# Kernel optimization log

Hardware: AMD Instinct MI355X
Metric: run time of the kernel (lower is better)

## Reference

```python
import jax, jax.numpy as jnp
import numpy as np

N = 100000   # relation nodes (== source nodes per scale)
D = 128      # per-scale feature size
EPS = 1e-6   # LayerNorm eps from the torch module


def setup_inputs() -> dict:
    key = jax.random.key(0)
    ks = jax.random.split(key, 10)
    inp = {}
    for i, s in enumerate(['s1', 's2', 's3', 's4']):
        inp[f'feat_{s}'] = jax.random.normal(ks[i], (N, D), dtype=jnp.float32)
        inp[f'idx_{s}'] = jax.random.randint(ks[4 + i], (N,), 0, N, dtype=jnp.int32)
    inp['W'] = jax.random.normal(ks[8], (4 * D, 4 * D), dtype=jnp.float32) * 0.04
    inp['b'] = jnp.zeros((4 * D,), dtype=jnp.float32)
    inp['gamma'] = jnp.ones((4 * D,), dtype=jnp.float32)
    inp['beta'] = jnp.zeros((4 * D,), dtype=jnp.float32)
    return inp


def reference(feat_s1, feat_s2, feat_s3, feat_s4,
              idx_s1, idx_s2, idx_s3, idx_s4,
              W, b, gamma, beta):
    # copy_src message passing per scale == gather src features to each
    # relation node (uniform in-degree 1), mailbox flatten -> [N, D] per scale.
    gathered = jnp.concatenate([
        jnp.take(feat_s1, idx_s1, axis=0),
        jnp.take(feat_s2, idx_s2, axis=0),
        jnp.take(feat_s3, idx_s3, axis=0),
        jnp.take(feat_s4, idx_s4, axis=0),
    ], axis=1)                                  # [N, 4D]
    h = gathered @ W.T + b                      # nn.Linear(4D, 4D)
    h = jax.nn.relu(h)
    # LayerNorm(4D, eps=1e-6, elementwise_affine=True)
    mu = jnp.mean(h, axis=-1, keepdims=True)
    var = jnp.mean(jnp.square(h - mu), axis=-1, keepdims=True)
    return (h - mu) * jax.lax.rsqrt(var + EPS) * gamma + beta
```

## Files before the change

### kernel.cpp

```cpp
#include <hip/hip_runtime.h>
#include <stdint.h>

#define N_ROWS 100000
#define EPS 1e-6f

typedef float f32x4 __attribute__((ext_vector_type(4)));
typedef __bf16 bf16x8 __attribute__((ext_vector_type(8)));
typedef ushort u16x8 __attribute__((ext_vector_type(8)));

__device__ __forceinline__ ushort f2bf(float f) {
  union { float f; uint32_t u; } v; v.f = f;
  uint32_t u = v.u;
  return (ushort)((u + 0x7FFFu + ((u >> 16) & 1u)) >> 16);
}

__global__ __launch_bounds__(256) void wconv2_kernel(const float* __restrict__ W,
                                                     ushort* __restrict__ Wf) {
  int t = blockIdx.x * 256 + threadIdx.x;
  int frag = t >> 6;
  int lane = t & 63;
  int j = (frag >> 4) * 16 + (lane & 15);
  int kb = (frag & 15) * 32 + (lane >> 4) * 8;
  const float* src = W + j * 512 + kb;
  float4 a = *(const float4*)src;
  float4 b = *(const float4*)(src + 4);
  ushort4 lo, hi;
  lo.x = f2bf(a.x); lo.y = f2bf(a.y); lo.z = f2bf(a.z); lo.w = f2bf(a.w);
  hi.x = f2bf(b.x); hi.y = f2bf(b.y); hi.z = f2bf(b.z); hi.w = f2bf(b.w);
  ushort* dst = Wf + (size_t)t * 8;
  *(ushort4*)dst = lo;
  *(ushort4*)(dst + 4) = hi;
}

__global__ __launch_bounds__(512, 4) void fused4_kernel(
    const float* __restrict__ f1, const float* __restrict__ f2,
    const float* __restrict__ f3, const float* __restrict__ f4,
    const int* __restrict__ i1, const int* __restrict__ i2,
    const int* __restrict__ i3, const int* __restrict__ i4,
    const ushort* __restrict__ Wf, const float* __restrict__ bias,
    const float* __restrict__ gamma, const float* __restrict__ beta,
    float* __restrict__ out) {
  __shared__ ushort Al[64 * 512];
  __shared__ float2 red[64 * 8];

  const int t = threadIdx.x;
  const int w = t >> 6;
  const int l = t & 63;
  const int cl = l & 15;
  const int gq = l >> 4;
  const int blk = blockIdx.x;

  const int arow = t >> 3;
  const int e8 = t & 7;
  int gi = blk * 64 + arow;
  int gic = gi < N_ROWS ? gi : (N_ROWS - 1);
  const float* tb0 = f1 + (size_t)i1[gic] * 128 + e8 * 8;
  const float* tb1 = f2 + (size_t)i2[gic] * 128 + e8 * 8;
  const float* tb2 = f3 + (size_t)i3[gic] * 128 + e8 * 8;
  const float* tb3 = f4 + (size_t)i4[gic] * 128 + e8 * 8;

  float4 pa[4][2], pb[4][2];
#pragma unroll
  for (int h = 0; h < 2; ++h) {
    pa[0][h] = *(const float4*)(tb0 + h * 64);
    pb[0][h] = *(const float4*)(tb0 + h * 64 + 4);
    pa[1][h] = *(const float4*)(tb1 + h * 64);
    pb[1][h] = *(const float4*)(tb1 + h * 64 + 4);
    pa[2][h] = *(const float4*)(tb2 + h * 64);
    pb[2][h] = *(const float4*)(tb2 + h * 64 + 4);
    pa[3][h] = *(const float4*)(tb3 + h * 64);
    pb[3][h] = *(const float4*)(tb3 + h * 64 + 4);
  }

#pragma unroll
  for (int T = 0; T < 4; ++T)
#pragma unroll
    for (int h = 0; h < 2; ++h) {
      u16x8 o;
      o[0] = f2bf(pa[T][h].x); o[1] = f2bf(pa[T][h].y);
      o[2] = f2bf(pa[T][h].z); o[3] = f2bf(pa[T][h].w);
      o[4] = f2bf(pb[T][h].x); o[5] = f2bf(pb[T][h].y);
      o[6] = f2bf(pb[T][h].z); o[7] = f2bf(pb[T][h].w);
      const int c = (T * 16 + h * 8 + e8) ^ (arow & 15);
      *(u16x8*)(Al + arow * 512 + c * 8) = o;
    }

  const ushort* Bbase = Wf + ((size_t)w * 4 * 16 * 64 + l) * 8;

  f32x4 acc[4][4];
#pragma unroll
  for (int rb = 0; rb < 4; ++rb)
#pragma unroll
    for (int cb = 0; cb < 4; ++cb)
      acc[rb][cb] = (f32x4){0.f, 0.f, 0.f, 0.f};

  __syncthreads();

#pragma unroll
  for (int kt = 0; kt < 16; ++kt) {
    bf16x8 bfr[4];
#pragma unroll
    for (int cb = 0; cb < 4; ++cb)
      bfr[cb] = *(const bf16x8*)(Bbase + ((size_t)cb * 16 + kt) * 512);
    bf16x8 af[4];
#pragma unroll
    for (int rb = 0; rb < 4; ++rb) {
      const int c = (kt * 4 + gq) ^ cl;
      af[rb] = *(const bf16x8*)(Al + (rb * 16 + cl) * 512 + c * 8);
    }
#pragma unroll
    for (int cb = 0; cb < 4; ++cb)
#pragma unroll
      for (int rb = 0; rb < 4; ++rb)
        acc[rb][cb] = __builtin_amdgcn_mfma_f32_16x16x32_bf16(
            af[rb], bfr[cb], acc[rb][cb], 0, 0, 0);
  }

  const int wcol = w * 64;
  float bia[4], gam[4], bet[4];
#pragma unroll
  for (int cb = 0; cb < 4; ++cb) {
    int col = wcol + cb * 16 + cl;
    bia[cb] = bias[col];
    gam[cb] = gamma[col];
    bet[cb] = beta[col];
  }

#pragma unroll
  for (int rb = 0; rb < 4; ++rb) {
#pragma unroll
    for (int r = 0; r < 4; ++r) {
      float s = 0.f, ss = 0.f;
#pragma unroll
      for (int cb = 0; cb < 4; ++cb) {
        float v = acc[rb][cb][r] + bia[cb];
        v = fmaxf(v, 0.f);
        acc[rb][cb][r] = v;
        s += v;
        ss += v * v;
      }
#pragma unroll
      for (int m = 1; m < 16; m <<= 1) {
        s += __shfl_xor(s, m);
        ss += __shfl_xor(ss, m);
      }
      if (cl == 0) {
        int row = rb * 16 + gq * 4 + r;
        red[row * 8 + w] = make_float2(s, ss);
      }
    }
  }
  __syncthreads();

#pragma unroll
  for (int rb = 0; rb < 4; ++rb) {
#pragma unroll
    for (int r = 0; r < 4; ++r) {
      int row = rb * 16 + gq * 4 + r;
      float S = 0.f, SS = 0.f;
#pragma unroll
      for (int wv = 0; wv < 8; ++wv) {
        float2 p = red[row * 8 + wv];
        S += p.x;
        SS += p.y;
      }
      float mu = S * (1.f / 512.f);
      float var = SS * (1.f / 512.f) - mu * mu;
      float rstd = rsqrtf(var + EPS);
      int g = blk * 64 + row;
      if (g < N_ROWS) {
        float* orow = out + (size_t)g * 512 + wcol;
#pragma unroll
        for (int cb = 0; cb < 4; ++cb)
          orow[cb * 16 + cl] = (acc[rb][cb][r] - mu) * rstd * gam[cb] + bet[cb];
      }
    }
  }
}

extern "C" void kernel_launch(void* const* d_in, const int* in_sizes, int n_in,
                              void* d_out, int out_size, void* d_ws, size_t ws_size,
                              hipStream_t stream) {
  const float* f1 = (const float*)d_in[0];
  const int* i1 = (const int*)d_in[1];
  const float* f2 = (const float*)d_in[2];
  const int* i2 = (const int*)d_in[3];
  const float* f3 = (const float*)d_in[4];
  const int* i3 = (const int*)d_in[5];
  const float* f4 = (const float*)d_in[6];
  const int* i4 = (const int*)d_in[7];
  const float* W = (const float*)d_in[8];
  const float* b = (const float*)d_in[9];
  const float* gm = (const float*)d_in[10];
  const float* bt = (const float*)d_in[11];
  float* out = (float*)d_out;
  ushort* Wf = (ushort*)d_ws;

  wconv2_kernel<<<128, 256, 0, stream>>>(W, Wf);
  fused4_kernel<<<(N_ROWS + 63) / 64, 512, 0, stream>>>(
      f1, f2, f3, f4, i1, i2, i3, i4, Wf, b, gm, bt, out);
}
```

Baseline: 174.2 us.

## Pipeline gathered A tiles through triple-buffered LDS chunks overlapping MFMA

The up-front gather of all 512 K-columns into a full 64x512 LDS tile is replaced by eight 64-column chunks. They are prefetched two ahead into registers and staged through a 3-slot LDS ring with a barrier per chunk. This overlaps the global gather latency with MFMA work and cuts LDS use from 64 KB to about 24 KB. The occupancy hint also drops from 4 to 3 blocks per CU, and the change adds eight barriers per block and more register pressure.

```diff
diff --git a/kernel.cpp b/kernel.cpp
--- a/kernel.cpp
+++ b/kernel.cpp
@@ -32,7 +32,7 @@
   *(ushort4*)(dst + 4) = hi;
 }
 
-__global__ __launch_bounds__(512, 4) void fused4_kernel(
+__global__ __launch_bounds__(512, 3) void fused5_kernel(
     const float* __restrict__ f1, const float* __restrict__ f2,
     const float* __restrict__ f3, const float* __restrict__ f4,
     const int* __restrict__ i1, const int* __restrict__ i2,
@@ -40,7 +40,7 @@
     const ushort* __restrict__ Wf, const float* __restrict__ bias,
     const float* __restrict__ gamma, const float* __restrict__ beta,
     float* __restrict__ out) {
-  __shared__ ushort Al[64 * 512];
+  __shared__ ushort Al[3][64 * 64];
   __shared__ float2 red[64 * 8];
 
   const int t = threadIdx.x;
@@ -54,36 +54,13 @@
   const int e8 = t & 7;
   int gi = blk * 64 + arow;
   int gic = gi < N_ROWS ? gi : (N_ROWS - 1);
-  const float* tb0 = f1 + (size_t)i1[gic] * 128 + e8 * 8;
-  const float* tb1 = f2 + (size_t)i2[gic] * 128 + e8 * 8;
-  const float* tb2 = f3 + (size_t)i3[gic] * 128 + e8 * 8;
-  const float* tb3 = f4 + (size_t)i4[gic] * 128 + e8 * 8;
-
-  float4 pa[4][2], pb[4][2];
-#pragma unroll
-  for (int h = 0; h < 2; ++h) {
-    pa[0][h] = *(const float4*)(tb0 + h * 64);
-    pb[0][h] = *(const float4*)(tb0 + h * 64 + 4);
-    pa[1][h] = *(const float4*)(tb1 + h * 64);
-    pb[1][h] = *(const float4*)(tb1 + h * 64 + 4);
-    pa[2][h] = *(const float4*)(tb2 + h * 64);
-    pb[2][h] = *(const float4*)(tb2 + h * 64 + 4);
-    pa[3][h] = *(const float4*)(tb3 + h * 64);
-    pb[3][h] = *(const float4*)(tb3 + h * 64 + 4);
-  }
-
-#pragma unroll
-  for (int T = 0; T < 4; ++T)
-#pragma unroll
-    for (int h = 0; h < 2; ++h) {
-      u16x8 o;
-      o[0] = f2bf(pa[T][h].x); o[1] = f2bf(pa[T][h].y);
-      o[2] = f2bf(pa[T][h].z); o[3] = f2bf(pa[T][h].w);
-      o[4] = f2bf(pb[T][h].x); o[5] = f2bf(pb[T][h].y);
-      o[6] = f2bf(pb[T][h].z); o[7] = f2bf(pb[T][h].w);
-      const int c = (T * 16 + h * 8 + e8) ^ (arow & 15);
-      *(u16x8*)(Al + arow * 512 + c * 8) = o;
-    }
+  const float* tp[4];
+  tp[0] = f1 + (size_t)i1[gic] * 128 + e8 * 8;
+  tp[1] = f2 + (size_t)i2[gic] * 128 + e8 * 8;
+  tp[2] = f3 + (size_t)i3[gic] * 128 + e8 * 8;
+  tp[3] = f4 + (size_t)i4[gic] * 128 + e8 * 8;
+
+  const int wboff = arow * 64 + ((e8 ^ (arow & 7)) * 8);
 
   const ushort* Bbase = Wf + ((size_t)w * 4 * 16 * 64 + l) * 8;
 
@@ -94,26 +71,62 @@
     for (int cb = 0; cb < 4; ++cb)
       acc[rb][cb] = (f32x4){0.f, 0.f, 0.f, 0.f};
 
-  __syncthreads();
-
-#pragma unroll
-  for (int kt = 0; kt < 16; ++kt) {
-    bf16x8 bfr[4];
-#pragma unroll
-    for (int cb = 0; cb < 4; ++cb)
-      bfr[cb] = *(const bf16x8*)(Bbase + ((size_t)cb * 16 + kt) * 512);
-    bf16x8 af[4];
-#pragma unroll
-    for (int rb = 0; rb < 4; ++rb) {
-      const int c = (kt * 4 + gq) ^ cl;
-      af[rb] = *(const bf16x8*)(Al + (rb * 16 + cl) * 512 + c * 8);
-    }
-#pragma unroll
-    for (int cb = 0; cb < 4; ++cb)
-#pragma unroll
-      for (int rb = 0; rb < 4; ++rb)
-        acc[rb][cb] = __builtin_amdgcn_mfma_f32_16x16x32_bf16(
-            af[rb], bfr[cb], acc[rb][cb], 0, 0, 0);
+  float4 pl[2][2];
+  pl[0][0] = *(const float4*)(tp[0]);
+  pl[0][1] = *(const float4*)(tp[0] + 4);
+  pl[1][0] = *(const float4*)(tp[0] + 64);
+  pl[1][1] = *(const float4*)(tp[0] + 68);
+  {
+    u16x8 o;
+    o[0] = f2bf(pl[0][0].x); o[1] = f2bf(pl[0][0].y);
+    o[2] = f2bf(pl[0][0].z); o[3] = f2bf(pl[0][0].w);
+    o[4] = f2bf(pl[0][1].x); o[5] = f2bf(pl[0][1].y);
+    o[6] = f2bf(pl[0][1].z); o[7] = f2bf(pl[0][1].w);
+    *(u16x8*)(Al[0] + wboff) = o;
+  }
+  asm volatile("s_waitcnt lgkmcnt(0)" ::: "memory");
+  __builtin_amdgcn_s_barrier();
+  asm volatile("" ::: "memory");
+
+#pragma unroll
+  for (int wi = 0; wi < 8; ++wi) {
+    if (wi + 2 < 8) {
+      const float* p = tp[(wi + 2) >> 1] + ((wi + 2) & 1) * 64;
+      pl[wi & 1][0] = *(const float4*)(p);
+      pl[wi & 1][1] = *(const float4*)(p + 4);
+    }
+    const ushort* As = Al[wi % 3];
+#pragma unroll
+    for (int s = 0; s < 2; ++s) {
+      const int kt = wi * 2 + s;
+      bf16x8 bfr[4];
+#pragma unroll
+      for (int cb = 0; cb < 4; ++cb)
+        bfr[cb] = *(const bf16x8*)(Bbase + ((size_t)(cb * 16 + kt)) * 512);
+      bf16x8 af[4];
+#pragma unroll
+      for (int rb = 0; rb < 4; ++rb) {
+        const int c = (s * 4 + gq) ^ (cl & 7);
+        af[rb] = *(const bf16x8*)(As + (rb * 16 + cl) * 64 + c * 8);
+      }
+#pragma unroll
+      for (int cb = 0; cb < 4; ++cb)
+#pragma unroll
+        for (int rb = 0; rb < 4; ++rb)
+          acc[rb][cb] = __builtin_amdgcn_mfma_f32_16x16x32_bf16(
+              af[rb], bfr[cb], acc[rb][cb], 0, 0, 0);
+    }
+    if (wi + 1 < 8) {
+      float4 qa = pl[(wi + 1) & 1][0];
+      float4 qb = pl[(wi + 1) & 1][1];
+      u16x8 o;
+      o[0] = f2bf(qa.x); o[1] = f2bf(qa.y); o[2] = f2bf(qa.z); o[3] = f2bf(qa.w);
+      o[4] = f2bf(qb.x); o[5] = f2bf(qb.y); o[6] = f2bf(qb.z); o[7] = f2bf(qb.w);
+      *(u16x8*)(Al[(wi + 1) % 3] + wboff) = o;
+      asm volatile("s_waitcnt lgkmcnt(0)" ::: "memory");
+      __builtin_amdgcn_s_barrier();
+      asm volatile("" ::: "memory");
+    }
   }
 
   const int wcol = w * 64;
@@ -197,6 +210,6 @@
   ushort* Wf = (ushort*)d_ws;
 
   wconv2_kernel<<<128, 256, 0, stream>>>(W, Wf);
-  fused4_kernel<<<(N_ROWS + 63) / 64, 512, 0, stream>>>(
+  fused5_kernel<<<(N_ROWS + 63) / 64, 512, 0, stream>>>(
       f1, f2, f3, f4, i1, i2, i3, i4, Wf, b, gm, bt, out);
 }
```

Measured after the change: 198.9 us. 1.14x slower.
